# Kernel tuning notes

Hardware: AMD Instinct MI355X
Metric: run time of the kernel (lower is better)

Reference implementation:

```python
import jax, jax.numpy as jnp
import numpy as np

EMBED_DIM = 2048
NUM_HEADS = 16
HEAD_DIM = EMBED_DIM // NUM_HEADS
WINDOW = 512          # sliding window size (inclusive: q - kv <= WINDOW)
CHUNK = WINDOW        # query chunk size; kv span per chunk = 2*CHUNK
SCALE = 1.0 / float(np.sqrt(HEAD_DIM))


def setup_inputs() -> dict:
    key = jax.random.key(0)
    k1, k2, k3 = jax.random.split(key, 3)
    B, S, E = 2, 4096, EMBED_DIM
    x = jax.random.normal(k1, (B, S, E), dtype=jnp.float32)
    # Linear weights, torch layout [out_features, in_features], small init for stability
    w_qkv = jax.random.normal(k2, (3 * E, E), dtype=jnp.float32) * (1.0 / np.sqrt(E))
    w_out = jax.random.normal(k3, (E, E), dtype=jnp.float32) * (1.0 / np.sqrt(E))
    return {"x": x, "w_qkv": w_qkv, "w_out": w_out}


def _sliding_window_attention(q, k, v):
    # q,k,v: [B,H,S,D]; causal + sliding-window (q_idx - kv_idx in [0, WINDOW])
    B, H, S, D = q.shape
    C = CHUNK
    nc = S // C
    qc = q.reshape(B, H, nc, C, D)                              # [B,H,nc,C,D]
    # pad one zero chunk in front of K/V so each query chunk sees (prev, cur)
    kp = jnp.pad(k, ((0, 0), (0, 0), (C, 0), (0, 0))).reshape(B, H, nc + 1, C, D)
    vp = jnp.pad(v, ((0, 0), (0, 0), (C, 0), (0, 0))).reshape(B, H, nc + 1, C, D)
    kc = jnp.concatenate([kp[:, :, :-1], kp[:, :, 1:]], axis=-2)  # [B,H,nc,2C,D]
    vc = jnp.concatenate([vp[:, :, :-1], vp[:, :, 1:]], axis=-2)  # [B,H,nc,2C,D]

    qa = jnp.arange(C)
    ka = jnp.arange(2 * C)
    diff = C + qa[:, None] - ka[None, :]                        # q_pos - kv_pos, [C,2C]
    base = (diff >= 0) & (diff <= WINDOW)                       # causal + window
    # mask out the zero-padding keys of the first chunk (global kv pos < 0)
    kv_pos = (jnp.arange(nc)[:, None] - 1) * C + ka[None, :]    # [nc,2C]
    mask = base[None, :, :] & (kv_pos >= 0)[:, None, :]         # [nc,C,2C]

    scores = jnp.einsum('bhncd,bhnkd->bhnck', qc, kc) * SCALE   # [B,H,nc,C,2C]
    scores = jnp.where(mask[None, None], scores, -jnp.inf)
    attn = jax.nn.softmax(scores, axis=-1)
    out = jnp.einsum('bhnck,bhnkd->bhncd', attn, vc)            # [B,H,nc,C,D]
    return out.reshape(B, H, S, D)


def reference(x, w_qkv, w_out):
    B, S, E = x.shape
    H, D = NUM_HEADS, HEAD_DIM
    qkv = x @ w_qkv.T                                           # [B,S,3E]
    qkv = qkv.reshape(B, S, 3, H, D).transpose(2, 0, 3, 1, 4)   # [3,B,H,S,D]
    q, k, v = qkv[0], qkv[1], qkv[2]
    o = _sliding_window_attention(q, k, v)                      # [B,H,S,D]
    o = o.transpose(0, 2, 1, 3).reshape(B, S, E)
    return o @ w_out.T
```

## Files before the change

kernel.cpp:

```cpp
#include <hip/hip_runtime.h>


typedef __bf16 bf16x8 __attribute__((ext_vector_type(8)));
typedef float  f32x4  __attribute__((ext_vector_type(4)));
typedef unsigned short u16x4 __attribute__((ext_vector_type(4)));

#define MFMA(a, b, c) __builtin_amdgcn_mfma_f32_16x16x32_bf16(a, b, c, 0, 0, 0)

__device__ __forceinline__ unsigned short f2bf(float f) {
  union { float f; unsigned u; } v; v.f = f;
  unsigned r = v.u + 0x7FFFu + ((v.u >> 16) & 1u);
  return (unsigned short)(r >> 16);
}

__device__ __forceinline__ void gl16(const void* g, void* l) {
  __builtin_amdgcn_global_load_lds(
      (const __attribute__((address_space(1))) unsigned int*)g,
      (__attribute__((address_space(3))) unsigned int*)l, 16, 0, 0);
}

__global__ void cast_bf16(const float4* __restrict__ in,
                          u16x4* __restrict__ out, int n4) {
  int i = blockIdx.x * blockDim.x + threadIdx.x;
  if (i < n4) {
    float4 v = in[i];
    u16x4 o;
    o[0] = f2bf(v.x); o[1] = f2bf(v.y); o[2] = f2bf(v.z); o[3] = f2bf(v.w);
    out[i] = o;
  }
}

template <int MODE>
__global__ __launch_bounds__(512, 2) void gemm_bt(
    const unsigned short* __restrict__ A, const unsigned short* __restrict__ Bw,
    void* __restrict__ C1, void* __restrict__ C2, int K, int Nstride) {
  __shared__ __align__(16) unsigned char sm[131072];
  const int tid = threadIdx.x, lane = tid & 63, w = tid >> 6;
  const int l15 = lane & 15, lg = lane >> 4;
  const int wr = w >> 2, wc = w & 3;

  int id = (int)blockIdx.x;
  int cpx = (int)gridDim.x >> 3;
  int sid = (id & 7) * cpx + (id >> 3);
  const int bm = (sid & 31) * 256;
  const int bn = (sid >> 5) * 256;

  f32x4 acc[8][4] = {};
  const int nt = K >> 5;

  const unsigned short* aRow0 = A  + (size_t)(bm + w * 16 + l15) * K + lg * 8;
  const unsigned short* aRow1 = A  + (size_t)(bm + (w + 8) * 16 + l15) * K + lg * 8;
  const unsigned short* bRow0 = Bw + (size_t)(bn + w * 16 + l15) * K + lg * 8;
  const unsigned short* bRow1 = Bw + (size_t)(bn + (w + 8) * 16 + l15) * K + lg * 8;

  auto stage = [&](int t) {
    int kt = ((t < nt) ? t : nt - 1) * 32;
    unsigned char* dst = sm + (t & 3) * 32768;
    gl16(aRow0 + kt, dst + w * 1024);
    gl16(aRow1 + kt, dst + (w + 8) * 1024);
    gl16(bRow0 + kt, dst + 16384 + w * 1024);
    gl16(bRow1 + kt, dst + 16384 + (w + 8) * 1024);
  };

  stage(0); stage(1); stage(2);
  asm volatile("s_waitcnt vmcnt(8)" ::: "memory");
  __builtin_amdgcn_s_barrier();

  for (int g = 0; g < nt; ++g) {
    unsigned char* cur = sm + (g & 3) * 32768;
    bf16x8 af[4], bfr[4];
#pragma unroll
    for (int i = 0; i < 4; i++)
      af[i] = *(const bf16x8*)(cur + (wr * 8 + i) * 1024 + lane * 16);
#pragma unroll
    for (int j = 0; j < 4; j++)
      bfr[j] = *(const bf16x8*)(cur + 16384 + (wc * 4 + j) * 1024 + lane * 16);
    __builtin_amdgcn_s_barrier();
    asm volatile("s_waitcnt lgkmcnt(0)" ::: "memory");
    __builtin_amdgcn_sched_barrier(0);
    __builtin_amdgcn_s_setprio(1);
#pragma unroll
    for (int i = 0; i < 4; i++)
#pragma unroll
      for (int j = 0; j < 4; j++)
        acc[i][j] = MFMA(af[i], bfr[j], acc[i][j]);
    __builtin_amdgcn_s_setprio(0);
#pragma unroll
    for (int i = 0; i < 4; i++)
      af[i] = *(const bf16x8*)(cur + (wr * 8 + 4 + i) * 1024 + lane * 16);
    stage(g + 3);
    asm volatile("s_waitcnt vmcnt(8)" ::: "memory");
    __builtin_amdgcn_s_barrier();
    asm volatile("s_waitcnt lgkmcnt(0)" ::: "memory");
    __builtin_amdgcn_sched_barrier(0);
    __builtin_amdgcn_s_setprio(1);
#pragma unroll
    for (int i = 0; i < 4; i++)
#pragma unroll
      for (int j = 0; j < 4; j++)
        acc[4 + i][j] = MFMA(af[i], bfr[j], acc[4 + i][j]);
    __builtin_amdgcn_s_setprio(0);
  }

  asm volatile("s_waitcnt vmcnt(0)" ::: "memory");

  if (MODE == 1) {
    unsigned short* QK = (unsigned short*)C1;
    unsigned short* VT = (unsigned short*)C2;
    if (bn < 4096) {
      const float scl = (bn < 2048) ? 0.08838834764831845f : 1.0f;
#pragma unroll
      for (int mi = 0; mi < 8; mi++) {
        int m0 = bm + wr * 128 + mi * 16 + lg * 4;
#pragma unroll
        for (int j = 0; j < 4; j++) {
          int n = bn + wc * 64 + j * 16 + l15;
#pragma unroll
          for (int r = 0; r < 4; r++)
            QK[(size_t)(m0 + r) * 4096 + n] = f2bf(acc[mi][j][r] * scl);
        }
      }
    } else {
#pragma unroll
      for (int mi = 0; mi < 8; mi++) {
        int m0 = bm + wr * 128 + mi * 16 + lg * 4;
        int bb = m0 >> 12, s = m0 & 4095;
#pragma unroll
        for (int j = 0; j < 4; j++) {
          int n4 = bn + wc * 64 + j * 16 + l15 - 4096;
          int hh = n4 >> 7, d = n4 & 127;
          u16x4 pk;
#pragma unroll
          for (int r = 0; r < 4; r++) pk[r] = f2bf(acc[mi][j][r]);
          *(u16x4*)(VT + ((size_t)((bb * 16 + hh) * 128 + d) * 4096 + s)) = pk;
        }
      }
    }
  } else {
    float* C = (float*)C1;
#pragma unroll
    for (int mi = 0; mi < 8; mi++) {
      int m0 = bm + wr * 128 + mi * 16 + lg * 4;
#pragma unroll
      for (int j = 0; j < 4; j++) {
        int n = bn + wc * 64 + j * 16 + l15;
#pragma unroll
        for (int r = 0; r < 4; r++)
          C[(size_t)(m0 + r) * Nstride + n] = acc[mi][j][r];
      }
    }
  }
}

__global__ __launch_bounds__(256, 2) void attn(
    const unsigned short* __restrict__ QK,
    const unsigned short* __restrict__ VT,
    unsigned short* __restrict__ O) {
  __shared__ unsigned char sm[67584];
  const int tid = threadIdx.x, lane = tid & 63, w = tid >> 6;
  const int l15 = lane & 15, lg = lane >> 4;
  const int bid = blockIdx.x;
  const int sid = (bid & 7) * 128 + (bid >> 3);
  const int qc = sid & 31, h = (sid >> 5) & 15, b = sid >> 9;
  const int q0 = qc * 128;

  bf16x8 qf[2][4];
#pragma unroll
  for (int mb = 0; mb < 2; mb++) {
    const unsigned short* qrow =
        QK + (size_t)(b * 4096 + q0 + (2 * w + mb) * 16 + l15) * 4096 + h * 128 + lg * 8;
#pragma unroll
    for (int ks = 0; ks < 4; ks++) qf[mb][ks] = *(const bf16x8*)(qrow + ks * 32);
  }

  float mrun[2] = {-1e30f, -1e30f}, lrun[2] = {0.f, 0.f};
  f32x4 oacc[8][2] = {};

  const int t0 = (q0 < 512) ? (512 - q0) >> 6 : 0;
  unsigned char* Ps = sm + 49152 + w * 4608;

  {
    const int kv0 = q0 - 512 + t0 * 64;
#pragma unroll
    for (int u = 0; u < 4; u++) {
      int f = w + u * 4;
      int kvb = f >> 2, ks = f & 3;
      gl16(QK + (size_t)(b * 4096 + kv0 + kvb * 16 + l15) * 4096 + 2048 + h * 128 + ks * 32 + lg * 8,
           sm + (t0 & 1) * 16384 + f * 1024);
      int db = f >> 1, kvs = f & 1;
      gl16(VT + (size_t)((b * 16 + h) * 128 + db * 16 + l15) * 4096 + kv0 + kvs * 32 + lg * 8,
           sm + 32768 + f * 1024);
    }
  }
  asm volatile("s_waitcnt vmcnt(0)" ::: "memory");
  __builtin_amdgcn_s_barrier();

  for (int t = t0; t < 10; t++) {
    const int kv0 = q0 - 512 + t * 64;
    const int X = t & 1;
    const int tn = (t + 1 < 10) ? t + 1 : 9;
    const int kvn = q0 - 512 + tn * 64;

#pragma unroll
    for (int u = 0; u < 4; u++) {
      int f = w + u * 4;
      int kvb = f >> 2, ks = f & 3;
      gl16(QK + (size_t)(b * 4096 + kvn + kvb * 16 + l15) * 4096 + 2048 + h * 128 + ks * 32 + lg * 8,
           sm + (X ^ 1) * 16384 + f * 1024);
    }

    f32x4 sacc[4][2] = {};
#pragma unroll
    for (int ks = 0; ks < 4; ks++)
#pragma unroll
      for (int kvb = 0; kvb < 4; kvb++) {
        bf16x8 kf = *(const bf16x8*)(sm + X * 16384 + (kvb * 4 + ks) * 1024 + lane * 16);
        sacc[kvb][0] = MFMA(kf, qf[0][ks], sacc[kvb][0]);
        sacc[kvb][1] = MFMA(kf, qf[1][ks], sacc[kvb][1]);
      }

    if (t <= 1 || t >= 8) {
#pragma unroll
      for (int kvb = 0; kvb < 4; kvb++)
#pragma unroll
        for (int mb = 0; mb < 2; mb++) {
          int qg = q0 + w * 32 + mb * 16 + l15;
          int kgb = kv0 + kvb * 16 + lg * 4;
#pragma unroll
          for (int r = 0; r < 4; r++) {
            int diff = qg - (kgb + r);
            if (diff < 0 || diff > 512) sacc[kvb][mb][r] = -1e30f;
          }
        }
    }

#pragma unroll
    for (int mb = 0; mb < 2; mb++) {
      float tmax = -1e30f;
#pragma unroll
      for (int kvb = 0; kvb < 4; kvb++)
#pragma unroll
        for (int r = 0; r < 4; r++) tmax = fmaxf(tmax, sacc[kvb][mb][r]);
      tmax = fmaxf(tmax, __shfl_xor(tmax, 16));
      tmax = fmaxf(tmax, __shfl_xor(tmax, 32));
      float mnew = fmaxf(mrun[mb], tmax);
      float alpha = __expf(mrun[mb] - mnew);
      mrun[mb] = mnew;
      float lsum = 0.f;
#pragma unroll
      for (int kvb = 0; kvb < 4; kvb++) {
        u16x4 pk;
#pragma unroll
        for (int r = 0; r < 4; r++) {
          float p = __expf(sacc[kvb][mb][r] - mnew);
          lsum += p;
          pk[r] = f2bf(p);
        }
        *(u16x4*)(Ps + (mb * 16 + l15) * 144 + kvb * 32 + lg * 8) = pk;
      }
      lsum += __shfl_xor(lsum, 16);
      lsum += __shfl_xor(lsum, 32);
      lrun[mb] = lrun[mb] * alpha + lsum;
#pragma unroll
      for (int db = 0; db < 8; db++)
#pragma unroll
        for (int r = 0; r < 4; r++) oacc[db][mb][r] *= alpha;
    }

    asm volatile("s_waitcnt vmcnt(4)" ::: "memory");
    __builtin_amdgcn_s_barrier();

#pragma unroll
    for (int kvs = 0; kvs < 2; kvs++) {
      bf16x8 pf0 = *(const bf16x8*)(Ps + (0 + l15) * 144 + kvs * 64 + lg * 16);
      bf16x8 pf1 = *(const bf16x8*)(Ps + (16 + l15) * 144 + kvs * 64 + lg * 16);
#pragma unroll
      for (int db = 0; db < 8; db++) {
        bf16x8 vf = *(const bf16x8*)(sm + 32768 + (db * 2 + kvs) * 1024 + lane * 16);
        oacc[db][0] = MFMA(vf, pf0, oacc[db][0]);
        oacc[db][1] = MFMA(vf, pf1, oacc[db][1]);
      }
    }
    __builtin_amdgcn_s_barrier();

#pragma unroll
    for (int u = 0; u < 4; u++) {
      int f = w + u * 4;
      int db = f >> 1, kvs = f & 1;
      gl16(VT + (size_t)((b * 16 + h) * 128 + db * 16 + l15) * 4096 + kvn + kvs * 32 + lg * 8,
           sm + 32768 + f * 1024);
    }
    asm volatile("s_waitcnt vmcnt(4)" ::: "memory");
    __builtin_amdgcn_s_barrier();
  }

  asm volatile("s_waitcnt vmcnt(0)" ::: "memory");

#pragma unroll
  for (int mb = 0; mb < 2; mb++) {
    float inv = 1.0f / lrun[mb];
    int s = q0 + w * 32 + mb * 16 + l15;
    unsigned short* orow = O + (size_t)(b * 4096 + s) * 2048 + h * 128 + lg * 4;
#pragma unroll
    for (int db = 0; db < 8; db++) {
      u16x4 pk;
#pragma unroll
      for (int r = 0; r < 4; r++) pk[r] = f2bf(oacc[db][mb][r] * inv);
      *(u16x4*)(orow + db * 16) = pk;
    }
  }
}

extern "C" void kernel_launch(void* const* d_in, const int* in_sizes, int n_in,
                              void* d_out, int out_size, void* d_ws, size_t ws_size,
                              hipStream_t stream) {
  const float* x = (const float*)d_in[0];
  const float* w_qkv = (const float*)d_in[1];
  const float* w_out = (const float*)d_in[2];
  float* out = (float*)d_out;

  char* ws = (char*)d_ws;
  unsigned short* XB    = (unsigned short*)(ws);
  unsigned short* WQKVB = (unsigned short*)(ws + 33554432);
  unsigned short* WOUTB = (unsigned short*)(ws + 58720256);
  unsigned short* QKb   = (unsigned short*)(ws + 67108864);
  unsigned short* VTb   = (unsigned short*)(ws + 134217728);
  unsigned short* OB    = XB;

  cast_bf16<<<16384, 256, 0, stream>>>((const float4*)x, (u16x4*)XB, 4194304);
  cast_bf16<<<12288, 256, 0, stream>>>((const float4*)w_qkv, (u16x4*)WQKVB, 3145728);
  cast_bf16<<<4096, 256, 0, stream>>>((const float4*)w_out, (u16x4*)WOUTB, 1048576);

  gemm_bt<1><<<768, 512, 0, stream>>>(XB, WQKVB, QKb, VTb, 2048, 0);

  attn<<<1024, 256, 0, stream>>>(QKb, VTb, OB);

  gemm_bt<2><<<256, 512, 0, stream>>>(OB, WOUTB, out, nullptr, 2048, 2048);
}
```

Before: 527.7 us.

## Use XOR-swizzled LDS layout and 64-wide K tiles in bf16 GEMM

Restructures the GEMM main loop to stage 64-wide K tiles as eight 16KB quarter slots. Global-to-LDS loads use an XOR swizzle on the column chunk, and the MFMA fragment reads use the matching swizzle to avoid LDS bank conflicts. The pipeline now prefetches one full tile ahead behind a __syncthreads instead of the earlier three-stage vmcnt-counted scheme. This cuts barriers per K element but may expose more global-load latency, because each iteration drains all outstanding loads.

```diff
diff --git a/kernel.cpp b/kernel.cpp
--- a/kernel.cpp
+++ b/kernel.cpp
@@ -39,6 +39,13 @@
   const int l15 = lane & 15, lg = lane >> 4;
   const int wr = w >> 2, wc = w & 3;
 
+  const int rr = lane >> 3;
+  const int cs = (((lane & 7) ^ rr) << 3);
+
+  const int r7 = l15 & 7;
+  const int mc0 = (l15 >> 3) * 1024 + r7 * 128 + ((lg ^ r7) << 4);
+  const int mc1 = (l15 >> 3) * 1024 + r7 * 128 + (((4 + lg) ^ r7) << 4);
+
   int id = (int)blockIdx.x;
   int cpx = (int)gridDim.x >> 3;
   int sid = (id & 7) * cpx + (id >> 3);
@@ -46,59 +53,64 @@
   const int bn = (sid >> 5) * 256;
 
   f32x4 acc[8][4] = {};
-  const int nt = K >> 5;
-
-  const unsigned short* aRow0 = A  + (size_t)(bm + w * 16 + l15) * K + lg * 8;
-  const unsigned short* aRow1 = A  + (size_t)(bm + (w + 8) * 16 + l15) * K + lg * 8;
-  const unsigned short* bRow0 = Bw + (size_t)(bn + w * 16 + l15) * K + lg * 8;
-  const unsigned short* bRow1 = Bw + (size_t)(bn + (w + 8) * 16 + l15) * K + lg * 8;
-
-  auto stage = [&](int t) {
-    int kt = ((t < nt) ? t : nt - 1) * 32;
-    unsigned char* dst = sm + (t & 3) * 32768;
-    gl16(aRow0 + kt, dst + w * 1024);
-    gl16(aRow1 + kt, dst + (w + 8) * 1024);
-    gl16(bRow0 + kt, dst + 16384 + w * 1024);
-    gl16(bRow1 + kt, dst + 16384 + (w + 8) * 1024);
+  const int nt = K >> 6;
+
+  auto stageQ = [&](int q) {
+    int qc = (q < 4 * nt) ? q : (4 * (nt - 1) + (q & 3));
+    int t = qc >> 2, part = qc & 3;
+    int kt = t << 6;
+    unsigned char* dst = sm + (q & 7) * 16384 + w * 2048;
+    const unsigned short* src =
+        (part < 2)
+            ? A  + (size_t)(bm + part * 128 + w * 16 + rr) * K + kt + cs
+            : Bw + (size_t)(bn + (part - 2) * 128 + w * 16 + rr) * K + kt + cs;
+    gl16(src, dst);
+    gl16(src + (size_t)8 * K, dst + 1024);
   };
 
-  stage(0); stage(1); stage(2);
-  asm volatile("s_waitcnt vmcnt(8)" ::: "memory");
-  __builtin_amdgcn_s_barrier();
+  stageQ(0); stageQ(1); stageQ(2); stageQ(3);
 
   for (int g = 0; g < nt; ++g) {
-    unsigned char* cur = sm + (g & 3) * 32768;
-    bf16x8 af[4], bfr[4];
-#pragma unroll
-    for (int i = 0; i < 4; i++)
-      af[i] = *(const bf16x8*)(cur + (wr * 8 + i) * 1024 + lane * 16);
+    __syncthreads();
+
+    stageQ((g << 2) + 4); stageQ((g << 2) + 5);
+    stageQ((g << 2) + 6); stageQ((g << 2) + 7);
+
+    const unsigned char* Abase = sm + ((((g << 2) + wr) & 7) << 14);
+    const unsigned char* Bbase =
+        sm + ((((g << 2) + 2 + (wc >> 1)) & 7) << 14) + ((wc & 1) << 13);
+    bf16x8 af[8], bfr[4];
+
+#pragma unroll
+    for (int i = 0; i < 8; i++)
+      af[i] = *(const bf16x8*)(Abase + i * 2048 + mc0);
 #pragma unroll
     for (int j = 0; j < 4; j++)
-      bfr[j] = *(const bf16x8*)(cur + 16384 + (wc * 4 + j) * 1024 + lane * 16);
-    __builtin_amdgcn_s_barrier();
+      bfr[j] = *(const bf16x8*)(Bbase + j * 2048 + mc0);
     asm volatile("s_waitcnt lgkmcnt(0)" ::: "memory");
     __builtin_amdgcn_sched_barrier(0);
     __builtin_amdgcn_s_setprio(1);
 #pragma unroll
-    for (int i = 0; i < 4; i++)
+    for (int i = 0; i < 8; i++)
 #pragma unroll
       for (int j = 0; j < 4; j++)
         acc[i][j] = MFMA(af[i], bfr[j], acc[i][j]);
     __builtin_amdgcn_s_setprio(0);
-#pragma unroll
-    for (int i = 0; i < 4; i++)
-      af[i] = *(const bf16x8*)(cur + (wr * 8 + 4 + i) * 1024 + lane * 16);
-    stage(g + 3);
-    asm volatile("s_waitcnt vmcnt(8)" ::: "memory");
-    __builtin_amdgcn_s_barrier();
+
+#pragma unroll
+    for (int i = 0; i < 8; i++)
+      af[i] = *(const bf16x8*)(Abase + i * 2048 + mc1);
+#pragma unroll
+    for (int j = 0; j < 4; j++)
+      bfr[j] = *(const bf16x8*)(Bbase + j * 2048 + mc1);
     asm volatile("s_waitcnt lgkmcnt(0)" ::: "memory");
     __builtin_amdgcn_sched_barrier(0);
     __builtin_amdgcn_s_setprio(1);
 #pragma unroll
-    for (int i = 0; i < 4; i++)
+    for (int i = 0; i < 8; i++)
 #pragma unroll
       for (int j = 0; j < 4; j++)
-        acc[4 + i][j] = MFMA(af[i], bfr[j], acc[4 + i][j]);
+        acc[i][j] = MFMA(af[i], bfr[j], acc[i][j]);
     __builtin_amdgcn_s_setprio(0);
   }
 
```

Result: faster. 483.7 us (-8.3%).
